# Performance work log

Hardware: AMD Instinct MI355X
Metric: run time of the kernel (lower is better)

Reference implementation:

```python
import jax, jax.numpy as jnp
import numpy as np

B, S, H = 8, 2048, 4096
N_SLOTS, MEM, RH = 64, 16, 256
TEMP = 1.0


def setup_inputs() -> dict:
    key = jax.random.key(0)
    ks = jax.random.split(key, 8)
    return {
        "embeds": jax.random.normal(ks[0], (B, S, H), jnp.float32),
        "hidden": jax.random.normal(ks[1], (B, S, H), jnp.float32),
        "W1": jax.random.normal(ks[2], (RH, H), jnp.float32) * (1.0 / np.sqrt(H)),
        "b1": jax.random.normal(ks[3], (RH,), jnp.float32) * 0.02,
        "W2": jax.random.normal(ks[4], (N_SLOTS, RH), jnp.float32) * (1.0 / np.sqrt(RH)),
        "b2": jax.random.normal(ks[5], (N_SLOTS,), jnp.float32) * 0.02,
        "gate_logits": jax.random.normal(ks[6], (N_SLOTS, MEM), jnp.float32),
        "memory": jax.random.normal(ks[7], (N_SLOTS, MEM, H), jnp.float32) * 0.02,
        "top_k": 4,
    }


def reference(embeds, hidden, W1, b1, W2, b2, gate_logits, memory, top_k):
    # Routing query: mean over sequence of token embeddings  [B,H]
    query = embeds.mean(axis=1)
    # Router MLP: Linear -> ReLU -> Linear, scaled by temperature  [B,N]
    h = jax.nn.relu(jnp.einsum("bh,rh->br", query, W1) + b1)
    logits = (jnp.einsum("br,nr->bn", h, W2) + b2) / TEMP
    # Top-k slot selection + softmax over selected logits
    top_vals, slot_ids = jax.lax.top_k(logits, top_k)        # [B,K]
    weights = jax.nn.softmax(top_vals, axis=-1)              # [B,K]
    # Per-slot contribution: sigmoid(gate) weighted sum over memory rows  [N,H]
    all_contribs = jnp.einsum("nm,nmh->nh", jax.nn.sigmoid(gate_logits), memory)
    # Gather selected slots and combine with routing weights  [B,H]
    selected = all_contribs[slot_ids]                        # [B,K,H]
    contrib = jnp.einsum("bk,bkh->bh", weights, selected)
    # Hook injection into last-layer hidden states  [B,S,H]
    return hidden + contrib[:, None, :]
```

## Files before the change

kernel.cpp:

```cpp
#include <hip/hip_runtime.h>
#include <hip/hip_bf16.h>
#include <math.h>

constexpr int B  = 8;
constexpr int S  = 2048;
constexpr int H  = 4096;
constexpr int N  = 64;
constexpr int MEM = 16;
constexpr int RH = 256;
constexpr int H4 = H / 4;
constexpr int SCHUNK = 16;

typedef float fx4 __attribute__((ext_vector_type(4)));

__device__ __forceinline__ float4 ntload4(const float4* p) {
    fx4 v = __builtin_nontemporal_load(reinterpret_cast<const fx4*>(p));
    return make_float4(v.x, v.y, v.z, v.w);
}
__device__ __forceinline__ void ntstore4(float4* p, float4 v) {
    fx4 w = {v.x, v.y, v.z, v.w};
    __builtin_nontemporal_store(w, reinterpret_cast<fx4*>(p));
}

__global__ __launch_bounds__(256) void k_partial(const float* __restrict__ embeds,
                                                 float* __restrict__ partial) {
    int blk = blockIdx.x;
    int c   = blk % SCHUNK;
    int ht  = (blk / SCHUNK) % (H4 / 256);
    int b   = blk / (SCHUNK * (H4 / 256));
    int h4  = ht * 256 + threadIdx.x;

    const float4* src = (const float4*)embeds + (size_t)b * S * H4 + h4;
    int s0 = c * (S / SCHUNK);
    float4 acc = {0.f, 0.f, 0.f, 0.f};
    #pragma unroll 8
    for (int s = 0; s < S / SCHUNK; ++s) {
        float4 v = ntload4(&src[(size_t)(s0 + s) * H4]);
        acc.x += v.x; acc.y += v.y; acc.z += v.z; acc.w += v.w;
    }
    ((float4*)partial)[((size_t)b * SCHUNK + c) * H4 + h4] = acc;
}

__global__ __launch_bounds__(256) void k_mean(const float* __restrict__ partial,
                                              float* __restrict__ q) {
    int i  = blockIdx.x * 256 + threadIdx.x;
    int b  = i / H4;
    int h4 = i % H4;
    const float4* p4 = (const float4*)partial;
    float4 acc = {0.f, 0.f, 0.f, 0.f};
    #pragma unroll
    for (int c = 0; c < SCHUNK; ++c) {
        float4 v = p4[((size_t)b * SCHUNK + c) * H4 + h4];
        acc.x += v.x; acc.y += v.y; acc.z += v.z; acc.w += v.w;
    }
    const float inv = 1.0f / (float)S;
    acc.x *= inv; acc.y *= inv; acc.z *= inv; acc.w *= inv;
    ((float4*)q)[i] = acc;
}

__global__ __launch_bounds__(256) void k_w1(const float* __restrict__ q,
                                            const float* __restrict__ W1,
                                            const float* __restrict__ b1,
                                            float* __restrict__ hws) {
    __shared__ float wred[4][B];
    int r = blockIdx.x, t = threadIdx.x;
    const float4* w4 = (const float4*)W1 + (size_t)r * H4;
    const float4* q4 = (const float4*)q;

    float acc[B];
    #pragma unroll
    for (int b = 0; b < B; ++b) acc[b] = 0.f;

    #pragma unroll
    for (int i = 0; i < H4 / 256; ++i) {
        int idx = i * 256 + t;
        float4 wv = ntload4(&w4[idx]);
        #pragma unroll
        for (int b = 0; b < B; ++b) {
            float4 qv = q4[(size_t)b * H4 + idx];
            acc[b] += wv.x * qv.x + wv.y * qv.y + wv.z * qv.z + wv.w * qv.w;
        }
    }
    #pragma unroll
    for (int b = 0; b < B; ++b) {
        float v = acc[b];
        #pragma unroll
        for (int off = 32; off > 0; off >>= 1) v += __shfl_down(v, off, 64);
        acc[b] = v;
    }
    int wave = t >> 6, lane = t & 63;
    if (lane == 0) {
        #pragma unroll
        for (int b = 0; b < B; ++b) wred[wave][b] = acc[b];
    }
    __syncthreads();
    if (t < B) {
        float s = wred[0][t] + wred[1][t] + wred[2][t] + wred[3][t] + b1[r];
        hws[(size_t)t * RH + r] = fmaxf(s, 0.0f);
    }
}

__global__ __launch_bounds__(64) void k_gate_contrib(const float* __restrict__ hws,
                                                     const float* __restrict__ W2,
                                                     const float* __restrict__ b2,
                                                     const float* __restrict__ gate,
                                                     const float* __restrict__ memory,
                                                     const int* __restrict__ topk_p,
                                                     float* __restrict__ contrib) {
    __shared__ float lh[RH];
    __shared__ float wf[64];

    int blk = blockIdx.x;
    int b   = blk / (H4 / 64);
    int ht  = blk % (H4 / 64);
    int lane = threadIdx.x;

    int K = topk_p[0];
    if (K > 8) K = 8;
    if (K < 1) K = 1;

    float4 hv = ((const float4*)hws)[(size_t)b * (RH / 4) + lane];
    lh[lane * 4 + 0] = hv.x; lh[lane * 4 + 1] = hv.y;
    lh[lane * 4 + 2] = hv.z; lh[lane * 4 + 3] = hv.w;
    __syncthreads();

    float logit;
    {
        const float4* w4 = (const float4*)W2 + (size_t)lane * (RH / 4);
        float acc = b2[lane];
        #pragma unroll 8
        for (int i = 0; i < RH / 4; ++i) {
            float4 wv = w4[i];
            acc += wv.x * lh[4 * i] + wv.y * lh[4 * i + 1] +
                   wv.z * lh[4 * i + 2] + wv.w * lh[4 * i + 3];
        }
        logit = acc;
    }

    float v = logit;
    float tvals[8]; int tids[8];
    #pragma unroll
    for (int k = 0; k < 8; ++k) {
        float m = v; int mi = lane;
        #pragma unroll
        for (int off = 32; off > 0; off >>= 1) {
            float om = __shfl_xor(m, off, 64);
            int   oi = __shfl_xor(mi, off, 64);
            if (om > m || (om == m && oi < mi)) { m = om; mi = oi; }
        }
        tvals[k] = m; tids[k] = mi;
        if (lane == mi) v = -INFINITY;
    }

    float mx = tvals[0];
    float e[8]; float se = 0.f;
    #pragma unroll
    for (int k = 0; k < 8; ++k) {
        float ek = (k < K) ? expf(tvals[k] - mx) : 0.f;
        e[k] = ek; se += ek;
    }
    float inv = 1.0f / se;

    {
        int k_of = lane >> 4, m_of = lane & 15;
        float wfv = 0.f;
        #pragma unroll
        for (int k = 0; k < 8; ++k) {
            if (k < K && k == k_of) {
                float g = gate[tids[k] * MEM + m_of];
                wfv = e[k] * inv / (1.0f + expf(-g));
            }
        }
        wf[lane] = wfv;
    }
    __syncthreads();

    int h4 = ht * 64 + lane;
    float4 a = {0.f, 0.f, 0.f, 0.f};
    #pragma unroll
    for (int k = 0; k < 8; ++k) {
        if (k < K) {
            const float4* mp = (const float4*)memory + ((size_t)tids[k] * MEM) * H4 + h4;
            #pragma unroll
            for (int m = 0; m < MEM; ++m) {
                float w = wf[k * MEM + m];
                float4 vv = mp[(size_t)m * H4];
                a.x += w * vv.x; a.y += w * vv.y; a.z += w * vv.z; a.w += w * vv.w;
            }
        }
    }
    ((float4*)contrib)[(size_t)b * H4 + h4] = a;
}

__global__ __launch_bounds__(256) void k_add(const float* __restrict__ hidden,
                                             const float* __restrict__ contrib,
                                             float* __restrict__ out) {
    const size_t total4 = (size_t)B * S * H4;
    const size_t stride = (size_t)gridDim.x * blockDim.x;
    const float4* hv4 = (const float4*)hidden;
    const float4* cv4 = (const float4*)contrib;
    float4* o4 = (float4*)out;
    for (size_t i = (size_t)blockIdx.x * blockDim.x + threadIdx.x; i < total4; i += stride) {
        int h4 = (int)(i & (size_t)(H4 - 1));
        int b  = (int)(i >> 21);
        float4 hv = ntload4(&hv4[i]);
        float4 cv = cv4[(size_t)b * H4 + h4];
        float4 o  = {hv.x + cv.x, hv.y + cv.y, hv.z + cv.z, hv.w + cv.w};
        ntstore4(&o4[i], o);
    }
}

extern "C" void kernel_launch(void* const* d_in, const int* in_sizes, int n_in,
                              void* d_out, int out_size, void* d_ws, size_t ws_size,
                              hipStream_t stream) {
    const float* embeds = (const float*)d_in[0];
    const float* hidden = (const float*)d_in[1];
    const float* W1     = (const float*)d_in[2];
    const float* b1     = (const float*)d_in[3];
    const float* W2     = (const float*)d_in[4];
    const float* b2     = (const float*)d_in[5];
    const float* gate   = (const float*)d_in[6];
    const float* memory = (const float*)d_in[7];
    const int*   topk   = (const int*)d_in[8];
    float* out = (float*)d_out;

    float* partial = (float*)d_ws;
    float* q       = partial + (size_t)B * SCHUNK * H;
    float* hws     = q       + (size_t)B * H;
    float* contrib = hws     + (size_t)B * RH;

    k_partial     <<<dim3(B * (H4 / 256) * SCHUNK), dim3(256), 0, stream>>>(embeds, partial);
    k_mean        <<<dim3(B * H4 / 256),            dim3(256), 0, stream>>>(partial, q);
    k_w1          <<<dim3(RH),                      dim3(256), 0, stream>>>(q, W1, b1, hws);
    k_gate_contrib<<<dim3(B * (H4 / 64)),           dim3(64),  0, stream>>>(hws, W2, b2, gate,
                                                                            memory, topk, contrib);
    k_add         <<<dim3(4096),                    dim3(256), 0, stream>>>(hidden, contrib, out);
}
```

Measured before the change: 161.7 us.

## Fuse pipeline into single cooperative kernel with grid-wide syncs

Merges the five separate launches (partial sum, mean, W1 layer, gate/top-k contribution, broadcast add) into one persistent cooperative kernel of 1024 blocks, separated by grid.sync barriers. It keeps a fallback to separate launches if the cooperative launch fails. The gate-contribution stage is also reshaped from 512 single-wave blocks to 32 blocks of 256 threads. The intent is to remove inter-kernel launch gaps. In exchange it adds four grid-wide barriers and idles most blocks during the small middle phases. The 32-block gather stage also has far less parallelism to hide memory latency.

```diff
diff --git a/kernel.cpp b/kernel.cpp
--- a/kernel.cpp
+++ b/kernel.cpp
@@ -1,15 +1,19 @@
 #include <hip/hip_runtime.h>
+#include <hip/hip_cooperative_groups.h>
 #include <hip/hip_bf16.h>
 #include <math.h>
+
+namespace cg = cooperative_groups;
 
 constexpr int B  = 8;
 constexpr int S  = 2048;
 constexpr int H  = 4096;
-constexpr int N  = 64;
+constexpr int NSLOT = 64;
 constexpr int MEM = 16;
 constexpr int RH = 256;
 constexpr int H4 = H / 4;
 constexpr int SCHUNK = 16;
+constexpr int GRID = 1024;
 
 typedef float fx4 __attribute__((ext_vector_type(4)));
 
@@ -22,14 +26,13 @@
     __builtin_nontemporal_store(w, reinterpret_cast<fx4*>(p));
 }
 
-__global__ __launch_bounds__(256) void k_partial(const float* __restrict__ embeds,
-                                                 float* __restrict__ partial) {
-    int blk = blockIdx.x;
+
+__device__ __forceinline__ void phase_partial(int blk, int t,
+        const float* __restrict__ embeds, float* __restrict__ partial) {
     int c   = blk % SCHUNK;
     int ht  = (blk / SCHUNK) % (H4 / 256);
     int b   = blk / (SCHUNK * (H4 / 256));
-    int h4  = ht * 256 + threadIdx.x;
-
+    int h4  = ht * 256 + t;
     const float4* src = (const float4*)embeds + (size_t)b * S * H4 + h4;
     int s0 = c * (S / SCHUNK);
     float4 acc = {0.f, 0.f, 0.f, 0.f};
@@ -41,9 +44,9 @@
     ((float4*)partial)[((size_t)b * SCHUNK + c) * H4 + h4] = acc;
 }
 
-__global__ __launch_bounds__(256) void k_mean(const float* __restrict__ partial,
-                                              float* __restrict__ q) {
-    int i  = blockIdx.x * 256 + threadIdx.x;
+__device__ __forceinline__ void phase_mean(int blk, int t,
+        const float* __restrict__ partial, float* __restrict__ q) {
+    int i  = blk * 256 + t;
     int b  = i / H4;
     int h4 = i % H4;
     const float4* p4 = (const float4*)partial;
@@ -58,12 +61,10 @@
     ((float4*)q)[i] = acc;
 }
 
-__global__ __launch_bounds__(256) void k_w1(const float* __restrict__ q,
-                                            const float* __restrict__ W1,
-                                            const float* __restrict__ b1,
-                                            float* __restrict__ hws) {
+__device__ __forceinline__ void phase_w1(int r, int t,
+        const float* __restrict__ q, const float* __restrict__ W1,
+        const float* __restrict__ b1, float* __restrict__ hws) {
     __shared__ float wred[4][B];
-    int r = blockIdx.x, t = threadIdx.x;
     const float4* w4 = (const float4*)W1 + (size_t)r * H4;
     const float4* q4 = (const float4*)q;
 
@@ -95,33 +96,24 @@
     }
     __syncthreads();
     if (t < B) {
-        float s = wred[0][t] + wred[1][t] + wred[2][t] + wred[3][t] + b1[r];
-        hws[(size_t)t * RH + r] = fmaxf(s, 0.0f);
-    }
-}
-
-__global__ __launch_bounds__(64) void k_gate_contrib(const float* __restrict__ hws,
-                                                     const float* __restrict__ W2,
-                                                     const float* __restrict__ b2,
-                                                     const float* __restrict__ gate,
-                                                     const float* __restrict__ memory,
-                                                     const int* __restrict__ topk_p,
-                                                     float* __restrict__ contrib) {
+        float s2 = wred[0][t] + wred[1][t] + wred[2][t] + wred[3][t] + b1[r];
+        hws[(size_t)t * RH + r] = fmaxf(s2, 0.0f);
+    }
+}
+
+__device__ __forceinline__ void phase_gate_contrib(int b, int ht, int t, int K,
+        const float* __restrict__ hws, const float* __restrict__ W2,
+        const float* __restrict__ b2, const float* __restrict__ gate,
+        const float* __restrict__ memory, float* __restrict__ contrib) {
     __shared__ float lh[RH];
-    __shared__ float wf[64];
-
-    int blk = blockIdx.x;
-    int b   = blk / (H4 / 64);
-    int ht  = blk % (H4 / 64);
-    int lane = threadIdx.x;
-
-    int K = topk_p[0];
-    if (K > 8) K = 8;
-    if (K < 1) K = 1;
-
-    float4 hv = ((const float4*)hws)[(size_t)b * (RH / 4) + lane];
-    lh[lane * 4 + 0] = hv.x; lh[lane * 4 + 1] = hv.y;
-    lh[lane * 4 + 2] = hv.z; lh[lane * 4 + 3] = hv.w;
+    __shared__ float wf[128];
+    int lane = t & 63;
+
+    if (t < 64) {
+        float4 hv = ((const float4*)hws)[(size_t)b * (RH / 4) + t];
+        lh[t * 4 + 0] = hv.x; lh[t * 4 + 1] = hv.y;
+        lh[t * 4 + 2] = hv.z; lh[t * 4 + 3] = hv.w;
+    }
     __syncthreads();
 
     float logit;
@@ -161,8 +153,8 @@
     }
     float inv = 1.0f / se;
 
-    {
-        int k_of = lane >> 4, m_of = lane & 15;
+    if (t < 128) {
+        int k_of = t >> 4, m_of = t & 15;
         float wfv = 0.f;
         #pragma unroll
         for (int k = 0; k < 8; ++k) {
@@ -171,11 +163,11 @@
                 wfv = e[k] * inv / (1.0f + expf(-g));
             }
         }
-        wf[lane] = wfv;
+        wf[t] = wfv;
     }
     __syncthreads();
 
-    int h4 = ht * 64 + lane;
+    int h4 = ht * 256 + t;
     float4 a = {0.f, 0.f, 0.f, 0.f};
     #pragma unroll
     for (int k = 0; k < 8; ++k) {
@@ -192,15 +184,14 @@
     ((float4*)contrib)[(size_t)b * H4 + h4] = a;
 }
 
-__global__ __launch_bounds__(256) void k_add(const float* __restrict__ hidden,
-                                             const float* __restrict__ contrib,
-                                             float* __restrict__ out) {
+__device__ __forceinline__ void phase_add(size_t gid, size_t gstride,
+        const float* __restrict__ hidden, const float* __restrict__ contrib,
+        float* __restrict__ out) {
     const size_t total4 = (size_t)B * S * H4;
-    const size_t stride = (size_t)gridDim.x * blockDim.x;
     const float4* hv4 = (const float4*)hidden;
     const float4* cv4 = (const float4*)contrib;
     float4* o4 = (float4*)out;
-    for (size_t i = (size_t)blockIdx.x * blockDim.x + threadIdx.x; i < total4; i += stride) {
+    for (size_t i = gid; i < total4; i += gstride) {
         int h4 = (int)(i & (size_t)(H4 - 1));
         int b  = (int)(i >> 21);
         float4 hv = ntload4(&hv4[i]);
@@ -208,6 +199,75 @@
         float4 o  = {hv.x + cv.x, hv.y + cv.y, hv.z + cv.z, hv.w + cv.w};
         ntstore4(&o4[i], o);
     }
+}
+
+__global__ __launch_bounds__(256, 4) void k_fused(
+        const float* __restrict__ embeds, const float* __restrict__ hidden,
+        const float* __restrict__ W1, const float* __restrict__ b1,
+        const float* __restrict__ W2, const float* __restrict__ b2,
+        const float* __restrict__ gate, const float* __restrict__ memory,
+        const int* __restrict__ topk_p,
+        float* __restrict__ partial, float* __restrict__ q,
+        float* __restrict__ hws, float* __restrict__ contrib,
+        float* __restrict__ out) {
+    cg::grid_group grid = cg::this_grid();
+    int blk = blockIdx.x, t = threadIdx.x;
+
+    if (blk < B * (H4 / 256) * SCHUNK)
+        phase_partial(blk, t, embeds, partial);
+    grid.sync();
+
+    if (blk < B * H4 / 256)
+        phase_mean(blk, t, partial, q);
+    grid.sync();
+
+    if (blk < RH)
+        phase_w1(blk, t, q, W1, b1, hws);
+    grid.sync();
+
+    if (blk < 32) {
+        int K = topk_p[0];
+        if (K > 8) K = 8;
+        if (K < 1) K = 1;
+        phase_gate_contrib(blk >> 2, blk & 3, t, K, hws, W2, b2, gate, memory, contrib);
+    }
+    grid.sync();
+
+    phase_add((size_t)blk * 256 + t, (size_t)GRID * 256, hidden, contrib, out);
+}
+
+__global__ __launch_bounds__(256) void k_partial_sa(const float* __restrict__ e,
+                                                    float* __restrict__ p) {
+    phase_partial(blockIdx.x, threadIdx.x, e, p);
+}
+__global__ __launch_bounds__(256) void k_mean_sa(const float* __restrict__ p,
+                                                 float* __restrict__ q) {
+    phase_mean(blockIdx.x, threadIdx.x, p, q);
+}
+__global__ __launch_bounds__(256) void k_w1_sa(const float* __restrict__ q,
+                                               const float* __restrict__ W1,
+                                               const float* __restrict__ b1,
+                                               float* __restrict__ hws) {
+    phase_w1(blockIdx.x, threadIdx.x, q, W1, b1, hws);
+}
+__global__ __launch_bounds__(256) void k_gc_sa(const float* __restrict__ hws,
+                                               const float* __restrict__ W2,
+                                               const float* __restrict__ b2,
+                                               const float* __restrict__ gate,
+                                               const float* __restrict__ memory,
+                                               const int* __restrict__ topk_p,
+                                               float* __restrict__ contrib) {
+    int K = topk_p[0];
+    if (K > 8) K = 8;
+    if (K < 1) K = 1;
+    phase_gate_contrib(blockIdx.x >> 2, blockIdx.x & 3, threadIdx.x, K,
+                       hws, W2, b2, gate, memory, contrib);
+}
+__global__ __launch_bounds__(256) void k_add_sa(const float* __restrict__ hidden,
+                                                const float* __restrict__ contrib,
+                                                float* __restrict__ out) {
+    phase_add((size_t)blockIdx.x * 256 + threadIdx.x,
+              (size_t)gridDim.x * 256, hidden, contrib, out);
 }
 
 extern "C" void kernel_launch(void* const* d_in, const int* in_sizes, int n_in,
@@ -229,10 +289,19 @@
     float* hws     = q       + (size_t)B * H;
     float* contrib = hws     + (size_t)B * RH;
 
-    k_partial     <<<dim3(B * (H4 / 256) * SCHUNK), dim3(256), 0, stream>>>(embeds, partial);
-    k_mean        <<<dim3(B * H4 / 256),            dim3(256), 0, stream>>>(partial, q);
-    k_w1          <<<dim3(RH),                      dim3(256), 0, stream>>>(q, W1, b1, hws);
-    k_gate_contrib<<<dim3(B * (H4 / 64)),           dim3(64),  0, stream>>>(hws, W2, b2, gate,
-                                                                            memory, topk, contrib);
-    k_add         <<<dim3(4096),                    dim3(256), 0, stream>>>(hidden, contrib, out);
-}
+    void* args[] = {(void*)&embeds, (void*)&hidden, (void*)&W1, (void*)&b1,
+                    (void*)&W2, (void*)&b2, (void*)&gate, (void*)&memory,
+                    (void*)&topk, (void*)&partial, (void*)&q, (void*)&hws,
+                    (void*)&contrib, (void*)&out};
+    hipError_t err = hipLaunchCooperativeKernel((const void*)k_fused,
+                                                dim3(GRID), dim3(256),
+                                                args, 0, stream);
+    if (err != hipSuccess) {
+        k_partial_sa<<<dim3(B * (H4 / 256) * SCHUNK), dim3(256), 0, stream>>>(embeds, partial);
+        k_mean_sa   <<<dim3(B * H4 / 256),            dim3(256), 0, stream>>>(partial, q);
+        k_w1_sa     <<<dim3(RH),                      dim3(256), 0, stream>>>(q, W1, b1, hws);
+        k_gc_sa     <<<dim3(32),                      dim3(256), 0, stream>>>(hws, W2, b2, gate,
+                                                                              memory, topk, contrib);
+        k_add_sa    <<<dim3(4096),                    dim3(256), 0, stream>>>(hidden, contrib, out);
+    }
+}
```

After: 556.5 us. 244% more time.

## Fuse routing and slot-contribution computation into the broadcast-add kernel

Applied to the files above, without the earlier changes.

Merges the gate/contribution kernel and the add kernel into one. Each 256-thread block recomputes the router logits, top-k, softmax weights and the gathered memory contribution for its H-tile, then streams 32 sequence rows of hidden into the output. This drops one launch and the contrib workspace round-trip. In exchange, routing and the memory gather are recomputed redundantly in each of 2048 blocks, which adds many L2 reads before the streaming loop starts.

```diff
diff --git a/kernel.cpp b/kernel.cpp
--- a/kernel.cpp
+++ b/kernel.cpp
@@ -5,7 +5,7 @@
 constexpr int B  = 8;
 constexpr int S  = 2048;
 constexpr int H  = 4096;
-constexpr int N  = 64;
+constexpr int NSLOT = 64;
 constexpr int MEM = 16;
 constexpr int RH = 256;
 constexpr int H4 = H / 4;
@@ -95,33 +95,34 @@
     }
     __syncthreads();
     if (t < B) {
-        float s = wred[0][t] + wred[1][t] + wred[2][t] + wred[3][t] + b1[r];
-        hws[(size_t)t * RH + r] = fmaxf(s, 0.0f);
-    }
-}
-
-__global__ __launch_bounds__(64) void k_gate_contrib(const float* __restrict__ hws,
-                                                     const float* __restrict__ W2,
-                                                     const float* __restrict__ b2,
-                                                     const float* __restrict__ gate,
-                                                     const float* __restrict__ memory,
-                                                     const int* __restrict__ topk_p,
-                                                     float* __restrict__ contrib) {
+        float s2 = wred[0][t] + wred[1][t] + wred[2][t] + wred[3][t] + b1[r];
+        hws[(size_t)t * RH + r] = fmaxf(s2, 0.0f);
+    }
+}
+
+__global__ __launch_bounds__(256) void k_add_mega(
+        const float* __restrict__ hidden, const float* __restrict__ hws,
+        const float* __restrict__ W2, const float* __restrict__ b2,
+        const float* __restrict__ gate, const float* __restrict__ memory,
+        const int* __restrict__ topk_p, float* __restrict__ out) {
     __shared__ float lh[RH];
-    __shared__ float wf[64];
+    __shared__ float wf[128];
 
     int blk = blockIdx.x;
-    int b   = blk / (H4 / 64);
-    int ht  = blk % (H4 / 64);
-    int lane = threadIdx.x;
+    int sb  = blk & 63;
+    int ht  = (blk >> 6) & 3;
+    int b   = blk >> 8;
+    int t   = threadIdx.x, lane = t & 63;
 
     int K = topk_p[0];
     if (K > 8) K = 8;
     if (K < 1) K = 1;
 
-    float4 hv = ((const float4*)hws)[(size_t)b * (RH / 4) + lane];
-    lh[lane * 4 + 0] = hv.x; lh[lane * 4 + 1] = hv.y;
-    lh[lane * 4 + 2] = hv.z; lh[lane * 4 + 3] = hv.w;
+    if (t < 64) {
+        float4 hv = ((const float4*)hws)[(size_t)b * (RH / 4) + t];
+        lh[t * 4 + 0] = hv.x; lh[t * 4 + 1] = hv.y;
+        lh[t * 4 + 2] = hv.z; lh[t * 4 + 3] = hv.w;
+    }
     __syncthreads();
 
     float logit;
@@ -161,8 +162,8 @@
     }
     float inv = 1.0f / se;
 
-    {
-        int k_of = lane >> 4, m_of = lane & 15;
+    if (t < 128) {
+        int k_of = t >> 4, m_of = t & 15;
         float wfv = 0.f;
         #pragma unroll
         for (int k = 0; k < 8; ++k) {
@@ -171,12 +172,12 @@
                 wfv = e[k] * inv / (1.0f + expf(-g));
             }
         }
-        wf[lane] = wfv;
+        wf[t] = wfv;
     }
     __syncthreads();
 
-    int h4 = ht * 64 + lane;
-    float4 a = {0.f, 0.f, 0.f, 0.f};
+    int h4 = ht * 256 + t;
+    float4 cv = {0.f, 0.f, 0.f, 0.f};
     #pragma unroll
     for (int k = 0; k < 8; ++k) {
         if (k < K) {
@@ -185,28 +186,20 @@
             for (int m = 0; m < MEM; ++m) {
                 float w = wf[k * MEM + m];
                 float4 vv = mp[(size_t)m * H4];
-                a.x += w * vv.x; a.y += w * vv.y; a.z += w * vv.z; a.w += w * vv.w;
+                cv.x += w * vv.x; cv.y += w * vv.y; cv.z += w * vv.z; cv.w += w * vv.w;
             }
         }
     }
-    ((float4*)contrib)[(size_t)b * H4 + h4] = a;
-}
-
-__global__ __launch_bounds__(256) void k_add(const float* __restrict__ hidden,
-                                             const float* __restrict__ contrib,
-                                             float* __restrict__ out) {
-    const size_t total4 = (size_t)B * S * H4;
-    const size_t stride = (size_t)gridDim.x * blockDim.x;
-    const float4* hv4 = (const float4*)hidden;
-    const float4* cv4 = (const float4*)contrib;
-    float4* o4 = (float4*)out;
-    for (size_t i = (size_t)blockIdx.x * blockDim.x + threadIdx.x; i < total4; i += stride) {
-        int h4 = (int)(i & (size_t)(H4 - 1));
-        int b  = (int)(i >> 21);
-        float4 hv = ntload4(&hv4[i]);
-        float4 cv = cv4[(size_t)b * H4 + h4];
+
+    const float4* hsrc = (const float4*)hidden + (size_t)b * S * H4
+                         + (size_t)(sb * 32) * H4 + h4;
+    float4* odst = (float4*)out + (size_t)b * S * H4
+                   + (size_t)(sb * 32) * H4 + h4;
+    #pragma unroll 4
+    for (int s = 0; s < 32; ++s) {
+        float4 hv = ntload4(&hsrc[(size_t)s * H4]);
         float4 o  = {hv.x + cv.x, hv.y + cv.y, hv.z + cv.z, hv.w + cv.w};
-        ntstore4(&o4[i], o);
+        ntstore4(&odst[(size_t)s * H4], o);
     }
 }
 
@@ -227,12 +220,10 @@
     float* partial = (float*)d_ws;
     float* q       = partial + (size_t)B * SCHUNK * H;
     float* hws     = q       + (size_t)B * H;
-    float* contrib = hws     + (size_t)B * RH;
-
-    k_partial     <<<dim3(B * (H4 / 256) * SCHUNK), dim3(256), 0, stream>>>(embeds, partial);
-    k_mean        <<<dim3(B * H4 / 256),            dim3(256), 0, stream>>>(partial, q);
-    k_w1          <<<dim3(RH),                      dim3(256), 0, stream>>>(q, W1, b1, hws);
-    k_gate_contrib<<<dim3(B * (H4 / 64)),           dim3(64),  0, stream>>>(hws, W2, b2, gate,
-                                                                            memory, topk, contrib);
-    k_add         <<<dim3(4096),                    dim3(256), 0, stream>>>(hidden, contrib, out);
-}
+
+    k_partial <<<dim3(B * (H4 / 256) * SCHUNK), dim3(256), 0, stream>>>(embeds, partial);
+    k_mean    <<<dim3(B * H4 / 256),            dim3(256), 0, stream>>>(partial, q);
+    k_w1      <<<dim3(RH),                      dim3(256), 0, stream>>>(q, W1, b1, hws);
+    k_add_mega<<<dim3(B * (H4 / 256) * (S / 32)), dim3(256), 0, stream>>>(hidden, hws, W2, b2,
+                                                                          gate, memory, topk, out);
+}
```

Measured after the change: 210.6 us. 30.2% more time.

## Fuse mean reduction into partial-sum kernel via atomic counters; widen gate/contrib blocks

Applied to the files above, without the earlier changes.

The separate mean kernel is removed. The last of the SCHUNK blocks in each group, detected through an atomic counter after a threadfence, sums the partials and writes the query, which saves one launch. The gate/contrib kernel moves from 64-thread blocks to 256-thread blocks with four times fewer blocks, so each block covers more of H for the router logits and top-k that every block recomputes. It adds a memset launch for the counters and an atomic-plus-fence sync step, and the fewer blocks in the contrib kernel may reduce parallelism.

```diff
diff --git a/kernel.cpp b/kernel.cpp
--- a/kernel.cpp
+++ b/kernel.cpp
@@ -5,11 +5,12 @@
 constexpr int B  = 8;
 constexpr int S  = 2048;
 constexpr int H  = 4096;
-constexpr int N  = 64;
+constexpr int NSLOT = 64;
 constexpr int MEM = 16;
 constexpr int RH = 256;
 constexpr int H4 = H / 4;
 constexpr int SCHUNK = 16;
+constexpr int NGROUP = B * (H4 / 256);
 
 typedef float fx4 __attribute__((ext_vector_type(4)));
 
@@ -22,12 +23,16 @@
     __builtin_nontemporal_store(w, reinterpret_cast<fx4*>(p));
 }
 
-__global__ __launch_bounds__(256) void k_partial(const float* __restrict__ embeds,
-                                                 float* __restrict__ partial) {
+__global__ __launch_bounds__(256) void k_partial_mean(const float* __restrict__ embeds,
+                                                      float* __restrict__ partial,
+                                                      float* __restrict__ q,
+                                                      unsigned int* __restrict__ counters) {
+    __shared__ unsigned int done;
     int blk = blockIdx.x;
     int c   = blk % SCHUNK;
-    int ht  = (blk / SCHUNK) % (H4 / 256);
-    int b   = blk / (SCHUNK * (H4 / 256));
+    int g   = blk / SCHUNK;
+    int ht  = g % (H4 / 256);
+    int b   = g / (H4 / 256);
     int h4  = ht * 256 + threadIdx.x;
 
     const float4* src = (const float4*)embeds + (size_t)b * S * H4 + h4;
@@ -39,23 +44,24 @@
         acc.x += v.x; acc.y += v.y; acc.z += v.z; acc.w += v.w;
     }
     ((float4*)partial)[((size_t)b * SCHUNK + c) * H4 + h4] = acc;
-}
-
-__global__ __launch_bounds__(256) void k_mean(const float* __restrict__ partial,
-                                              float* __restrict__ q) {
-    int i  = blockIdx.x * 256 + threadIdx.x;
-    int b  = i / H4;
-    int h4 = i % H4;
-    const float4* p4 = (const float4*)partial;
-    float4 acc = {0.f, 0.f, 0.f, 0.f};
-    #pragma unroll
-    for (int c = 0; c < SCHUNK; ++c) {
-        float4 v = p4[((size_t)b * SCHUNK + c) * H4 + h4];
-        acc.x += v.x; acc.y += v.y; acc.z += v.z; acc.w += v.w;
-    }
-    const float inv = 1.0f / (float)S;
-    acc.x *= inv; acc.y *= inv; acc.z *= inv; acc.w *= inv;
-    ((float4*)q)[i] = acc;
+
+    __threadfence();
+    if (threadIdx.x == 0) done = atomicAdd(&counters[g], 1u);
+    __syncthreads();
+
+    if (done == SCHUNK - 1) {
+        __threadfence();
+        const float4* p4 = (const float4*)partial;
+        float4 s2 = {0.f, 0.f, 0.f, 0.f};
+        #pragma unroll
+        for (int c2 = 0; c2 < SCHUNK; ++c2) {
+            float4 v = p4[((size_t)b * SCHUNK + c2) * H4 + h4];
+            s2.x += v.x; s2.y += v.y; s2.z += v.z; s2.w += v.w;
+        }
+        const float inv = 1.0f / (float)S;
+        s2.x *= inv; s2.y *= inv; s2.z *= inv; s2.w *= inv;
+        ((float4*)q)[(size_t)b * H4 + h4] = s2;
+    }
 }
 
 __global__ __launch_bounds__(256) void k_w1(const float* __restrict__ q,
@@ -95,33 +101,34 @@
     }
     __syncthreads();
     if (t < B) {
-        float s = wred[0][t] + wred[1][t] + wred[2][t] + wred[3][t] + b1[r];
-        hws[(size_t)t * RH + r] = fmaxf(s, 0.0f);
-    }
-}
-
-__global__ __launch_bounds__(64) void k_gate_contrib(const float* __restrict__ hws,
-                                                     const float* __restrict__ W2,
-                                                     const float* __restrict__ b2,
-                                                     const float* __restrict__ gate,
-                                                     const float* __restrict__ memory,
-                                                     const int* __restrict__ topk_p,
-                                                     float* __restrict__ contrib) {
+        float s2 = wred[0][t] + wred[1][t] + wred[2][t] + wred[3][t] + b1[r];
+        hws[(size_t)t * RH + r] = fmaxf(s2, 0.0f);
+    }
+}
+
+__global__ __launch_bounds__(256) void k_gc(const float* __restrict__ hws,
+                                            const float* __restrict__ W2,
+                                            const float* __restrict__ b2,
+                                            const float* __restrict__ gate,
+                                            const float* __restrict__ memory,
+                                            const int* __restrict__ topk_p,
+                                            float* __restrict__ contrib) {
     __shared__ float lh[RH];
-    __shared__ float wf[64];
-
+    __shared__ float wf[128];
     int blk = blockIdx.x;
-    int b   = blk / (H4 / 64);
-    int ht  = blk % (H4 / 64);
-    int lane = threadIdx.x;
+    int b   = blk >> 2;
+    int ht  = blk & 3;
+    int t   = threadIdx.x, lane = t & 63;
 
     int K = topk_p[0];
     if (K > 8) K = 8;
     if (K < 1) K = 1;
 
-    float4 hv = ((const float4*)hws)[(size_t)b * (RH / 4) + lane];
-    lh[lane * 4 + 0] = hv.x; lh[lane * 4 + 1] = hv.y;
-    lh[lane * 4 + 2] = hv.z; lh[lane * 4 + 3] = hv.w;
+    if (t < 64) {
+        float4 hv = ((const float4*)hws)[(size_t)b * (RH / 4) + t];
+        lh[t * 4 + 0] = hv.x; lh[t * 4 + 1] = hv.y;
+        lh[t * 4 + 2] = hv.z; lh[t * 4 + 3] = hv.w;
+    }
     __syncthreads();
 
     float logit;
@@ -161,8 +168,8 @@
     }
     float inv = 1.0f / se;
 
-    {
-        int k_of = lane >> 4, m_of = lane & 15;
+    if (t < 128) {
+        int k_of = t >> 4, m_of = t & 15;
         float wfv = 0.f;
         #pragma unroll
         for (int k = 0; k < 8; ++k) {
@@ -171,11 +178,11 @@
                 wfv = e[k] * inv / (1.0f + expf(-g));
             }
         }
-        wf[lane] = wfv;
-    }
-    __syncthreads();
-
-    int h4 = ht * 64 + lane;
+        wf[t] = wfv;
+    }
+    __syncthreads();
+
+    int h4 = ht * 256 + t;
     float4 a = {0.f, 0.f, 0.f, 0.f};
     #pragma unroll
     for (int k = 0; k < 8; ++k) {
@@ -228,11 +235,13 @@
     float* q       = partial + (size_t)B * SCHUNK * H;
     float* hws     = q       + (size_t)B * H;
     float* contrib = hws     + (size_t)B * RH;
-
-    k_partial     <<<dim3(B * (H4 / 256) * SCHUNK), dim3(256), 0, stream>>>(embeds, partial);
-    k_mean        <<<dim3(B * H4 / 256),            dim3(256), 0, stream>>>(partial, q);
-    k_w1          <<<dim3(RH),                      dim3(256), 0, stream>>>(q, W1, b1, hws);
-    k_gate_contrib<<<dim3(B * (H4 / 64)),           dim3(64),  0, stream>>>(hws, W2, b2, gate,
-                                                                            memory, topk, contrib);
-    k_add         <<<dim3(4096),                    dim3(256), 0, stream>>>(hidden, contrib, out);
-}
+    unsigned int* counters = (unsigned int*)(contrib + (size_t)B * H);
+
+    hipMemsetAsync(counters, 0, NGROUP * sizeof(unsigned int), stream);
+
+    k_partial_mean<<<dim3(NGROUP * SCHUNK), dim3(256), 0, stream>>>(embeds, partial, q, counters);
+    k_w1          <<<dim3(RH),              dim3(256), 0, stream>>>(q, W1, b1, hws);
+    k_gc          <<<dim3(NGROUP),          dim3(256), 0, stream>>>(hws, W2, b2, gate,
+                                                                    memory, topk, contrib);
+    k_add         <<<dim3(4096),            dim3(256), 0, stream>>>(hidden, contrib, out);
+}
```

New measurement: 263.4 us. 62.9% more time.
